# Optimization experiments

Measured on AMD Instinct MI355X. Metric: run time of the kernel, lower is better.

The kernel has to match this reference:

```python
import jax, jax.numpy as jnp
import numpy as np

N_NODES = 50000
N_EDGES = 800000
IN_F = 191
H1, C1 = 16, 16   # conv1: heads=16, out=16, concat -> 256
H2, C2 = 8, 3     # conv2: heads=8, out=3, concat=False -> mean


def _glorot(key, shape):
    fan = shape[0] + shape[-1] if len(shape) == 2 else sum(shape)
    s = jnp.sqrt(6.0 / fan)
    return jax.random.uniform(key, shape, jnp.float32, -s, s)


def setup_inputs() -> dict:
    key = jax.random.key(0)
    ks = jax.random.split(key, 16)
    x = jax.random.normal(ks[0], (N_NODES, IN_F), jnp.float32)
    edge_index = jax.random.randint(ks[1], (2, N_EDGES), 0, N_NODES)
    edge_attr = jax.random.normal(ks[2], (N_EDGES, 1), jnp.float32)
    return {
        "x": x, "edge_index": edge_index, "edge_attr": edge_attr,
        "W1": _glorot(ks[3], (IN_F, H1 * C1)),
        "We1": _glorot(ks[4], (1, H1 * C1)),
        "a_src1": _glorot(ks[5], (H1, C1)),
        "a_dst1": _glorot(ks[6], (H1, C1)),
        "a_edge1": _glorot(ks[7], (H1, C1)),
        "b1": jnp.zeros((H1 * C1,), jnp.float32),
        "W2": _glorot(ks[8], (H1 * C1, H2 * C2)),
        "We2": _glorot(ks[9], (1, H2 * C2)),
        "a_src2": _glorot(ks[10], (H2, C2)),
        "a_dst2": _glorot(ks[11], (H2, C2)),
        "a_edge2": _glorot(ks[12], (H2, C2)),
        "b2": jnp.zeros((C2,), jnp.float32),
    }


def gat_conv(x, src, dst, edge_attr, W, We, a_src, a_dst, a_edge, bias, H, C, concat):
    # x: [N, F]; src/dst: [E'] (self loops already appended); edge_attr: [E', De]
    N = x.shape[0]
    xl = (x @ W).reshape(N, H, C)                       # [N,H,C]
    e = (edge_attr @ We).reshape(-1, H, C)              # [E',H,C]
    alpha_src = (xl * a_src).sum(-1)                    # [N,H]
    alpha_dst = (xl * a_dst).sum(-1)                    # [N,H]
    alpha_e = (e * a_edge).sum(-1)                      # [E',H]
    alpha = alpha_src[src] + alpha_dst[dst] + alpha_e   # [E',H]
    alpha = jax.nn.leaky_relu(alpha, 0.2)
    # softmax over incoming edges per destination node
    m = jax.ops.segment_max(alpha, dst, num_segments=N)
    alpha = jnp.exp(alpha - m[dst])
    den = jax.ops.segment_sum(alpha, dst, num_segments=N)
    alpha = alpha / (den[dst] + 1e-16)
    out = jax.ops.segment_sum(alpha[:, :, None] * xl[src], dst, num_segments=N)  # [N,H,C]
    if concat:
        return out.reshape(N, H * C) + bias
    return out.mean(axis=1) + bias


def reference(x, edge_index, edge_attr, W1, We1, a_src1, a_dst1, a_edge1, b1,
              W2, We2, a_src2, a_dst2, a_edge2, b2):
    N = x.shape[0]
    # add self loops (PyG default, edge_attr fill_value='mean')
    loop = jnp.arange(N)
    src = jnp.concatenate([edge_index[0], loop])
    dst = jnp.concatenate([edge_index[1], loop])
    ea_mean = edge_attr.mean(axis=0, keepdims=True)
    ea = jnp.concatenate([edge_attr, jnp.broadcast_to(ea_mean, (N, edge_attr.shape[1]))], axis=0)

    h = gat_conv(x, src, dst, ea, W1, We1, a_src1, a_dst1, a_edge1, b1, H1, C1, True)
    h = jax.nn.elu(h)
    h = gat_conv(h, src, dst, ea, W2, We2, a_src2, a_dst2, a_edge2, b2, H2, C2, False)
    h = jax.nn.elu(h)
    return h
```

## Files before the change

### kernel.cpp

```cpp
#include <hip/hip_runtime.h>
#include <math.h>
#include <stdint.h>

#define N_NODES 50000
#define N_EDGES 800000
#define N_TOT   850000
#define IN_F    191
#define F1      256
#define NH1     16
#define NC1     16
#define F2      24
#define NH2     8
#define NC2     3
#define KP      192
#define MPAD    50048
#define NCVT_X  (MPAD * 24)
#define NCVT_W  (F1 * 24)

typedef __attribute__((ext_vector_type(8))) short bf16x8;
typedef __attribute__((ext_vector_type(4))) float f32x4;

#define GLL16(g, s) __builtin_amdgcn_global_load_lds( \
    (const __attribute__((address_space(1))) void*)(g), \
    (__attribute__((address_space(3))) void*)(s), 16, 0, 0)

__device__ __forceinline__ float lrelu(float x) { return x > 0.f ? x : 0.2f * x; }

__device__ __forceinline__ uint16_t f2bf1(float f) {
    uint32_t u = __float_as_uint(f);
    return (uint16_t)((u + 0x7fffu + ((u >> 16) & 1u)) >> 16);
}
__device__ __forceinline__ uint16_t f2bf(float f, float* back) {
    uint32_t u = __float_as_uint(f);
    uint32_t r = (u + 0x7fffu + ((u >> 16) & 1u)) >> 16;
    *back = __uint_as_float(r << 16);
    return (uint16_t)r;
}
__device__ __forceinline__ void bf2f2(uint32_t u, float* lo, float* hi) {
    *lo = __uint_as_float(u << 16);
    *hi = __uint_as_float(u & 0xffff0000u);
}

__global__ void k_hist(const int* __restrict__ ei, int* counts) {
    int e = blockIdx.x * blockDim.x + threadIdx.x;
    if (e < N_EDGES) atomicAdd(&counts[ei[N_EDGES + e]], 1);
}

__global__ void k_easum(const float* __restrict__ ea, float* scalars) {
    __shared__ float wsums[4];
    int t = threadIdx.x;
    float v = 0.f;
    for (int e = blockIdx.x * 256 + t; e < N_EDGES; e += 256 * 256) v += ea[e];
    #pragma unroll
    for (int off = 32; off >= 1; off >>= 1) v += __shfl_xor(v, off);
    if ((t & 63) == 0) wsums[t >> 6] = v;
    __syncthreads();
    if (t == 0) atomicAdd(&scalars[25], wsums[0] + wsums[1] + wsums[2] + wsums[3]);
}

__global__ void k_wedot(const float* __restrict__ We1, const float* __restrict__ ae1,
                        const float* __restrict__ We2, const float* __restrict__ ae2,
                        float* scalars) {
    int t = threadIdx.x;
    if (t < NH1) {
        float s = 0.f;
        for (int c = 0; c < NC1; c++) s += We1[t * NC1 + c] * ae1[t * NC1 + c];
        scalars[1 + t] = s;
    } else if (t < NH1 + NH2) {
        int h = t - NH1;
        float s = 0.f;
        for (int c = 0; c < NC2; c++) s += We2[h * NC2 + c] * ae2[h * NC2 + c];
        scalars[17 + h] = s;
    } else if (t == 63) {
        scalars[0] = scalars[25] / (float)N_EDGES;
    }
}

__global__ __launch_bounds__(1024) void k_scan1(const int* __restrict__ counts,
                                                int* rowptr, int* bsums) {
    __shared__ int wsum[16];
    int t = threadIdx.x;
    int lane = t & 63, w = t >> 6;
    int i = blockIdx.x * 1024 + t;
    int v = (i < N_NODES) ? counts[i] + 1 : 0;
    int incl = v;
    #pragma unroll
    for (int off = 1; off < 64; off <<= 1) {
        int u = __shfl_up(incl, off);
        if (lane >= off) incl += u;
    }
    if (lane == 63) wsum[w] = incl;
    __syncthreads();
    int woff = 0;
    #pragma unroll
    for (int k = 0; k < 16; k++) woff += (k < w) ? wsum[k] : 0;
    if (i < N_NODES) rowptr[i] = woff + incl - v;
    if (t == 1023) bsums[blockIdx.x] = woff + incl;
}

__global__ __launch_bounds__(1024) void k_scan2(int* rowptr, int* cursor,
                                                const int* __restrict__ bsums) {
    __shared__ int off_s;
    int b = blockIdx.x, t = threadIdx.x;
    if (t == 0) {
        int o = 0;
        for (int k = 0; k < b; k++) o += bsums[k];
        off_s = o;
        if (b == 48) rowptr[N_NODES] = o + bsums[48];
    }
    __syncthreads();
    int i = b * 1024 + t;
    if (i < N_NODES) {
        int r = rowptr[i] + off_s;
        rowptr[i] = r;
        cursor[i] = r;
    }
}

__global__ void k_scatter(const int* __restrict__ ei, const float* __restrict__ ea,
                          const float* __restrict__ scalars, int* cursor,
                          uint2* __restrict__ csr) {
    int i = blockIdx.x * blockDim.x + threadIdx.x;
    if (i < N_EDGES) {
        int s = ei[i], d = ei[N_EDGES + i];
        int pos = atomicAdd(&cursor[d], 1);
        csr[pos] = make_uint2((uint32_t)s, __float_as_uint(ea[i]));
    } else if (i < N_TOT) {
        int n = i - N_EDGES;
        int pos = atomicAdd(&cursor[n], 1);
        csr[pos] = make_uint2((uint32_t)n, __float_as_uint(scalars[0]));
    }
}

__global__ void k_cvt(const float* __restrict__ x, const float* __restrict__ W1,
                      uint16_t* __restrict__ xh, uint16_t* __restrict__ xl,
                      uint16_t* __restrict__ wht, uint16_t* __restrict__ wlt) {
    int idx = blockIdx.x * 256 + threadIdx.x;
    if (idx < NCVT_X) {
        int row = idx / 24, kw = idx - row * 24;
        int k0 = kw * 8;
        uint16_t hv[8], lv[8];
        #pragma unroll
        for (int j = 0; j < 8; j++) {
            int k = k0 + j;
            float v = (row < N_NODES && k < IN_F) ? x[(size_t)row * IN_F + k] : 0.f;
            float hf;
            hv[j] = f2bf(v, &hf);
            lv[j] = f2bf1(v - hf);
        }
        *(uint4*)(xh + (size_t)row * KP + k0) = *(const uint4*)hv;
        *(uint4*)(xl + (size_t)row * KP + k0) = *(const uint4*)lv;
    } else if (idx < NCVT_X + NCVT_W) {
        int id2 = idx - NCVT_X;
        int col = id2 / 24, kw = id2 - col * 24;
        int k0 = kw * 8;
        uint16_t hv[8], lv[8];
        #pragma unroll
        for (int j = 0; j < 8; j++) {
            int k = k0 + j;
            float v = (k < IN_F) ? W1[(size_t)k * F1 + col] : 0.f;
            float hf;
            hv[j] = f2bf(v, &hf);
            lv[j] = f2bf1(v - hf);
        }
        *(uint4*)(wht + (size_t)col * KP + k0) = *(const uint4*)hv;
        *(uint4*)(wlt + (size_t)col * KP + k0) = *(const uint4*)lv;
    }
}

__global__ __launch_bounds__(256) void k_gemm1_mfma(const uint16_t* __restrict__ xh,
        const uint16_t* __restrict__ xl, const uint16_t* __restrict__ wht,
        const uint16_t* __restrict__ wlt, uint16_t* __restrict__ xl1b) {
    __shared__ uint16_t lds[4 * 8 * 64 * 8];
    const int t = threadIdx.x;
    const int l = t & 63, w = t >> 6;
    const int wm = w >> 1, wn = w & 1;
    const int m0 = blockIdx.x * 128;
    const int n0 = blockIdx.y * 128;
    const int lr = l & 15, lk = l >> 4;

    uint16_t* ldsAh = lds;
    uint16_t* ldsAl = lds + 8 * 64 * 8;
    uint16_t* ldsBh = lds + 2 * 8 * 64 * 8;
    uint16_t* ldsBl = lds + 3 * 8 * 64 * 8;

    f32x4 acc[4][4];
    #pragma unroll
    for (int i = 0; i < 4; i++)
        #pragma unroll
        for (int j = 0; j < 4; j++)
            acc[i][j] = (f32x4){0.f, 0.f, 0.f, 0.f};

    for (int ks = 0; ks < 6; ks++) {
        const int kb = ks * 32 + lk * 8;
        #pragma unroll
        for (int ii = 0; ii < 2; ii++) {
            const int f = 2 * w + ii;
            const uint16_t* sAh = xh  + (size_t)(m0 + f * 16 + lr) * KP + kb;
            const uint16_t* sAl = xl  + (size_t)(m0 + f * 16 + lr) * KP + kb;
            const uint16_t* sBh = wht + (size_t)(n0 + f * 16 + lr) * KP + kb;
            const uint16_t* sBl = wlt + (size_t)(n0 + f * 16 + lr) * KP + kb;
            GLL16(sAh, ldsAh + f * 512);
            GLL16(sAl, ldsAl + f * 512);
            GLL16(sBh, ldsBh + f * 512);
            GLL16(sBl, ldsBl + f * 512);
        }
        __syncthreads();
        bf16x8 ah[4], al[4];
        #pragma unroll
        for (int i = 0; i < 4; i++) {
            const int f = wm * 4 + i;
            ah[i] = *(const bf16x8*)(ldsAh + (f * 64 + l) * 8);
            al[i] = *(const bf16x8*)(ldsAl + (f * 64 + l) * 8);
        }
        #pragma unroll
        for (int j = 0; j < 4; j++) {
            const int g = wn * 4 + j;
            bf16x8 bh = *(const bf16x8*)(ldsBh + (g * 64 + l) * 8);
            bf16x8 bl = *(const bf16x8*)(ldsBl + (g * 64 + l) * 8);
            #pragma unroll
            for (int i = 0; i < 4; i++) {
                acc[i][j] = __builtin_amdgcn_mfma_f32_16x16x32_bf16(ah[i], bh, acc[i][j], 0, 0, 0);
                acc[i][j] = __builtin_amdgcn_mfma_f32_16x16x32_bf16(ah[i], bl, acc[i][j], 0, 0, 0);
                acc[i][j] = __builtin_amdgcn_mfma_f32_16x16x32_bf16(al[i], bh, acc[i][j], 0, 0, 0);
            }
        }
        __syncthreads();
    }
    #pragma unroll
    for (int i = 0; i < 4; i++) {
        const int gm_base = m0 + wm * 64 + i * 16 + lk * 4;
        #pragma unroll
        for (int r = 0; r < 4; r++) {
            const int gm = gm_base + r;
            if (gm < N_NODES) {
                #pragma unroll
                for (int j = 0; j < 4; j++) {
                    const int gn = n0 + wn * 64 + j * 16 + lr;
                    xl1b[(size_t)gm * F1 + gn] = f2bf1(acc[i][j][r]);
                }
            }
        }
    }
}

__global__ void k_alphas1(const uint16_t* __restrict__ xl1b, const float* __restrict__ a_src,
                          const float* __restrict__ a_dst,
                          float* __restrict__ asrc, float* __restrict__ adst) {
    int idx = blockIdx.x * blockDim.x + threadIdx.x;
    if (idx >= N_NODES * NH1) return;
    int h = idx & 15;
    const uint4* xp = (const uint4*)(xl1b + (size_t)idx * 16);
    uint4 u0 = xp[0], u1 = xp[1];
    uint32_t us[8] = {u0.x, u0.y, u0.z, u0.w, u1.x, u1.y, u1.z, u1.w};
    float as = 0.f, ad = 0.f;
    #pragma unroll
    for (int q = 0; q < 8; q++) {
        float lo, hi;
        bf2f2(us[q], &lo, &hi);
        as += lo * a_src[h * 16 + 2 * q] + hi * a_src[h * 16 + 2 * q + 1];
        ad += lo * a_dst[h * 16 + 2 * q] + hi * a_dst[h * 16 + 2 * q + 1];
    }
    asrc[idx] = as;
    adst[idx] = ad;
}

__global__ __launch_bounds__(256) void k_agg1(const int* __restrict__ rowptr,
        const uint2* __restrict__ csr,
        const uint16_t* __restrict__ xl1b, const float* __restrict__ asrc,
        const float* __restrict__ adst, const float* __restrict__ scalars,
        const float* __restrict__ b1, uint16_t* __restrict__ h1b) {
    int node = blockIdx.x * 4 + (threadIdx.x >> 6);
    int lane = threadIdx.x & 63;
    int eg = lane >> 4, h = lane & 15;
    int r0 = rowptr[node], r1 = rowptr[node + 1];
    float ad = adst[node * 16 + h];
    float wd = scalars[1 + h];
    float den = 0.f;
    float acc[16];
    #pragma unroll
    for (int c = 0; c < 16; c++) acc[c] = 0.f;
    for (int j = r0 + eg; j < r1; j += 4) {
        uint2 pk = csr[j];
        int s = (int)pk.x;
        float a = lrelu(asrc[s * 16 + h] + ad + __uint_as_float(pk.y) * wd);
        float wgt = __expf(a);
        den += wgt;
        const uint4* xp = (const uint4*)(xl1b + (size_t)s * F1 + h * 16);
        uint4 u0 = xp[0], u1 = xp[1];
        float lo, hi;
        bf2f2(u0.x, &lo, &hi); acc[0] += wgt * lo;  acc[1] += wgt * hi;
        bf2f2(u0.y, &lo, &hi); acc[2] += wgt * lo;  acc[3] += wgt * hi;
        bf2f2(u0.z, &lo, &hi); acc[4] += wgt * lo;  acc[5] += wgt * hi;
        bf2f2(u0.w, &lo, &hi); acc[6] += wgt * lo;  acc[7] += wgt * hi;
        bf2f2(u1.x, &lo, &hi); acc[8] += wgt * lo;  acc[9] += wgt * hi;
        bf2f2(u1.y, &lo, &hi); acc[10] += wgt * lo; acc[11] += wgt * hi;
        bf2f2(u1.z, &lo, &hi); acc[12] += wgt * lo; acc[13] += wgt * hi;
        bf2f2(u1.w, &lo, &hi); acc[14] += wgt * lo; acc[15] += wgt * hi;
    }
    den += __shfl_xor(den, 16);
    den += __shfl_xor(den, 32);
    float inv = 1.f / (den + 1e-16f);
    #pragma unroll
    for (int c = 0; c < 16; c++) {
        acc[c] += __shfl_xor(acc[c], 16);
        acc[c] += __shfl_xor(acc[c], 32);
    }
    if (eg == 0) {
        uint32_t pk[8];
        #pragma unroll
        for (int q = 0; q < 8; q++) {
            float v0 = acc[2 * q] * inv + b1[h * 16 + 2 * q];
            float v1 = acc[2 * q + 1] * inv + b1[h * 16 + 2 * q + 1];
            v0 = v0 > 0.f ? v0 : expm1f(v0);
            v1 = v1 > 0.f ? v1 : expm1f(v1);
            pk[q] = (uint32_t)f2bf1(v0) | ((uint32_t)f2bf1(v1) << 16);
        }
        uint4* op = (uint4*)(h1b + (size_t)node * F1 + h * 16);
        op[0] = make_uint4(pk[0], pk[1], pk[2], pk[3]);
        op[1] = make_uint4(pk[4], pk[5], pk[6], pk[7]);
    }
}

__global__ __launch_bounds__(256) void k_layer2(const uint16_t* __restrict__ h1b,
        const float* __restrict__ W2, const float* __restrict__ a_src,
        const float* __restrict__ a_dst, uint16_t* __restrict__ xl2b,
        float* __restrict__ asrc, float* __restrict__ adst) {
    __shared__ float W2s[F2][258];
    int t = threadIdx.x;
    for (int i = t; i < 256 * F2; i += 256) {
        int k = i / F2, c = i - k * F2;
        W2s[c][k] = W2[i];
    }
    __syncthreads();
    int idx = blockIdx.x * 256 + t;
    if (idx >= N_NODES * NH2) return;
    int n = idx >> 3, h = idx & 7;
    int c0 = h * 3;
    const uint4* hp = (const uint4*)(h1b + (size_t)n * F1);
    float a0 = 0.f, a1 = 0.f, a2 = 0.f;
    #pragma unroll 4
    for (int q = 0; q < 32; q++) {
        uint4 u = hp[q];
        float f[8];
        bf2f2(u.x, &f[0], &f[1]);
        bf2f2(u.y, &f[2], &f[3]);
        bf2f2(u.z, &f[4], &f[5]);
        bf2f2(u.w, &f[6], &f[7]);
        #pragma unroll
        for (int j = 0; j < 8; j++) {
            int k = q * 8 + j;
            a0 += f[j] * W2s[c0][k];
            a1 += f[j] * W2s[c0 + 1][k];
            a2 += f[j] * W2s[c0 + 2][k];
        }
    }
    uint2 pk;
    pk.x = (uint32_t)f2bf1(a0) | ((uint32_t)f2bf1(a1) << 16);
    pk.y = (uint32_t)f2bf1(a2);
    *(uint2*)(xl2b + (size_t)idx * 4) = pk;
    asrc[idx] = a0 * a_src[h * 3 + 0] + a1 * a_src[h * 3 + 1] + a2 * a_src[h * 3 + 2];
    adst[idx] = a0 * a_dst[h * 3 + 0] + a1 * a_dst[h * 3 + 1] + a2 * a_dst[h * 3 + 2];
}

__global__ __launch_bounds__(256) void k_agg2(const int* __restrict__ rowptr,
        const uint2* __restrict__ csr,
        const uint16_t* __restrict__ xl2b, const float* __restrict__ asrc,
        const float* __restrict__ adst, const float* __restrict__ scalars,
        const float* __restrict__ b2, float* __restrict__ out) {
    int node = blockIdx.x * 4 + (threadIdx.x >> 6);
    int lane = threadIdx.x & 63;
    int eg = lane >> 3, h = lane & 7;
    int r0 = rowptr[node], r1 = rowptr[node + 1];
    float ad = adst[node * 8 + h];
    float wd = scalars[17 + h];
    float den = 0.f, a0 = 0.f, a1 = 0.f, a2 = 0.f;
    for (int j = r0 + eg; j < r1; j += 8) {
        uint2 pk = csr[j];
        int s = (int)pk.x;
        float a = lrelu(asrc[s * 8 + h] + ad + __uint_as_float(pk.y) * wd);
        float wgt = __expf(a);
        den += wgt;
        const uint2* xp = (const uint2*)(xl2b + ((size_t)s * 8 + h) * 4);
        uint2 u = xp[0];
        float x0, x1, x2, dummy;
        bf2f2(u.x, &x0, &x1);
        bf2f2(u.y, &x2, &dummy);
        a0 += wgt * x0;
        a1 += wgt * x1;
        a2 += wgt * x2;
    }
    den += __shfl_xor(den, 8); den += __shfl_xor(den, 16); den += __shfl_xor(den, 32);
    float inv = 1.f / (den + 1e-16f);
    a0 += __shfl_xor(a0, 8); a0 += __shfl_xor(a0, 16); a0 += __shfl_xor(a0, 32);
    a1 += __shfl_xor(a1, 8); a1 += __shfl_xor(a1, 16); a1 += __shfl_xor(a1, 32);
    a2 += __shfl_xor(a2, 8); a2 += __shfl_xor(a2, 16); a2 += __shfl_xor(a2, 32);
    a0 *= inv; a1 *= inv; a2 *= inv;
    a0 += __shfl_xor(a0, 1); a0 += __shfl_xor(a0, 2); a0 += __shfl_xor(a0, 4);
    a1 += __shfl_xor(a1, 1); a1 += __shfl_xor(a1, 2); a1 += __shfl_xor(a1, 4);
    a2 += __shfl_xor(a2, 1); a2 += __shfl_xor(a2, 2); a2 += __shfl_xor(a2, 4);
    if (lane == 0) {
        float v0 = a0 * 0.125f + b2[0];
        float v1 = a1 * 0.125f + b2[1];
        float v2 = a2 * 0.125f + b2[2];
        out[node * 3 + 0] = v0 > 0.f ? v0 : expm1f(v0);
        out[node * 3 + 1] = v1 > 0.f ? v1 : expm1f(v1);
        out[node * 3 + 2] = v2 > 0.f ? v2 : expm1f(v2);
    }
}

extern "C" void kernel_launch(void* const* d_in, const int* in_sizes, int n_in,
                              void* d_out, int out_size, void* d_ws, size_t ws_size,
                              hipStream_t stream) {
    const float* x       = (const float*)d_in[0];
    const int*   ei      = (const int*)d_in[1];
    const float* ea      = (const float*)d_in[2];
    const float* W1      = (const float*)d_in[3];
    const float* We1     = (const float*)d_in[4];
    const float* a_src1  = (const float*)d_in[5];
    const float* a_dst1  = (const float*)d_in[6];
    const float* a_edge1 = (const float*)d_in[7];
    const float* b1      = (const float*)d_in[8];
    const float* W2      = (const float*)d_in[9];
    const float* We2     = (const float*)d_in[10];
    const float* a_src2  = (const float*)d_in[11];
    const float* a_dst2  = (const float*)d_in[12];
    const float* a_edge2 = (const float*)d_in[13];
    const float* b2      = (const float*)d_in[14];
    float* out = (float*)d_out;

    char* ws = (char*)d_ws;
    size_t off = 0;
    auto alloc = [&](size_t nbytes) -> void* {
        void* p = ws + off;
        off = (off + nbytes + 255) & ~(size_t)255;
        return p;
    };
    uint16_t* xl1b = (uint16_t*)alloc((size_t)N_NODES * F1 * 2);
    uint16_t* h1b  = (uint16_t*)alloc((size_t)N_NODES * F1 * 2);
    float* asrc1   = (float*)alloc((size_t)N_NODES * NH1 * 4);
    float* adst1   = (float*)alloc((size_t)N_NODES * NH1 * 4);
    uint16_t* xl2b = (uint16_t*)alloc((size_t)N_NODES * 32 * 2);
    float* asrc2   = (float*)alloc((size_t)N_NODES * NH2 * 4);
    float* adst2   = (float*)alloc((size_t)N_NODES * NH2 * 4);
    int*   counts  = (int*)alloc((size_t)N_NODES * 4);
    int*   rowptr  = (int*)alloc((size_t)(N_NODES + 1) * 4);
    int*   cursor  = (int*)alloc((size_t)N_NODES * 4);
    int*   bsums   = (int*)alloc(64 * 4);
    uint2* csr     = (uint2*)alloc((size_t)N_TOT * 8);
    float* scalars = (float*)alloc(128);
    uint16_t* wht  = (uint16_t*)alloc((size_t)F1 * KP * 2);
    uint16_t* wlt  = (uint16_t*)alloc((size_t)F1 * KP * 2);
    uint16_t* xh   = (uint16_t*)alloc((size_t)MPAD * KP * 2);
    uint16_t* xlo  = (uint16_t*)alloc((size_t)MPAD * KP * 2);

    hipMemsetAsync(counts, 0, (size_t)N_NODES * 4, stream);
    hipMemsetAsync(scalars, 0, 128, stream);
    hipLaunchKernelGGL(k_hist, dim3((N_EDGES + 255) / 256), dim3(256), 0, stream,
                       ei, counts);
    hipLaunchKernelGGL(k_easum, dim3(256), dim3(256), 0, stream, ea, scalars);
    hipLaunchKernelGGL(k_wedot, dim3(1), dim3(64), 0, stream,
                       We1, a_edge1, We2, a_edge2, scalars);
    hipLaunchKernelGGL(k_scan1, dim3(49), dim3(1024), 0, stream, counts, rowptr, bsums);
    hipLaunchKernelGGL(k_scan2, dim3(49), dim3(1024), 0, stream, rowptr, cursor, bsums);
    hipLaunchKernelGGL(k_scatter, dim3((N_TOT + 255) / 256), dim3(256), 0, stream,
                       ei, ea, scalars, cursor, csr);
    hipLaunchKernelGGL(k_cvt, dim3((NCVT_X + NCVT_W + 255) / 256), dim3(256), 0, stream,
                       x, W1, xh, xlo, wht, wlt);
    hipLaunchKernelGGL(k_gemm1_mfma, dim3(MPAD / 128, 2), dim3(256), 0, stream,
                       xh, xlo, wht, wlt, xl1b);
    hipLaunchKernelGGL(k_alphas1, dim3((N_NODES * NH1 + 255) / 256), dim3(256), 0, stream,
                       xl1b, a_src1, a_dst1, asrc1, adst1);
    hipLaunchKernelGGL(k_agg1, dim3(N_NODES / 4), dim3(256), 0, stream,
                       rowptr, csr, xl1b, asrc1, adst1, scalars, b1, h1b);
    hipLaunchKernelGGL(k_layer2, dim3((N_NODES * NH2 + 255) / 256), dim3(256), 0, stream,
                       h1b, W2, a_src2, a_dst2, xl2b, asrc2, adst2);
    hipLaunchKernelGGL(k_agg2, dim3(N_NODES / 4), dim3(256), 0, stream,
                       rowptr, csr, xl2b, asrc2, adst2, scalars, b2, out);
}
```

Baseline: 327.8 us.

## Slice layer-1 features into 32-column planes and aggregate per slice for cache locality

Stores the layer-1 transformed features and hidden output as eight [N,32] bf16 slices, and runs aggregation as eight passes over edges, one per slice. Each pass's random gathers hit a small working set that can stay cached. The GEMM is retiled to 64-row blocks covering all 256 columns and writes the sliced layout; alphas and layer-2 readers are adapted. The trade-off is that CSR and attention inputs are reread eight times and each gather is narrower.

```diff
diff --git a/kernel.cpp b/kernel.cpp
--- a/kernel.cpp
+++ b/kernel.cpp
@@ -170,19 +170,15 @@
 
 __global__ __launch_bounds__(256) void k_gemm1_mfma(const uint16_t* __restrict__ xh,
         const uint16_t* __restrict__ xl, const uint16_t* __restrict__ wht,
-        const uint16_t* __restrict__ wlt, uint16_t* __restrict__ xl1b) {
-    __shared__ uint16_t lds[4 * 8 * 64 * 8];
+        const uint16_t* __restrict__ wlt, uint16_t* __restrict__ xl1s) {
+    __shared__ uint16_t Ah[4 * 64 * 8];
+    __shared__ uint16_t Al[4 * 64 * 8];
+    __shared__ uint16_t Bh[16 * 64 * 8];
+    __shared__ uint16_t Bl[16 * 64 * 8];
     const int t = threadIdx.x;
     const int l = t & 63, w = t >> 6;
-    const int wm = w >> 1, wn = w & 1;
-    const int m0 = blockIdx.x * 128;
-    const int n0 = blockIdx.y * 128;
+    const int m0 = blockIdx.x * 64;
     const int lr = l & 15, lk = l >> 4;
-
-    uint16_t* ldsAh = lds;
-    uint16_t* ldsAl = lds + 8 * 64 * 8;
-    uint16_t* ldsBh = lds + 2 * 8 * 64 * 8;
-    uint16_t* ldsBl = lds + 3 * 8 * 64 * 8;
 
     f32x4 acc[4][4];
     #pragma unroll
@@ -194,63 +190,69 @@
     for (int ks = 0; ks < 6; ks++) {
         const int kb = ks * 32 + lk * 8;
         #pragma unroll
-        for (int ii = 0; ii < 2; ii++) {
-            const int f = 2 * w + ii;
-            const uint16_t* sAh = xh  + (size_t)(m0 + f * 16 + lr) * KP + kb;
-            const uint16_t* sAl = xl  + (size_t)(m0 + f * 16 + lr) * KP + kb;
-            const uint16_t* sBh = wht + (size_t)(n0 + f * 16 + lr) * KP + kb;
-            const uint16_t* sBl = wlt + (size_t)(n0 + f * 16 + lr) * KP + kb;
-            GLL16(sAh, ldsAh + f * 512);
-            GLL16(sAl, ldsAl + f * 512);
-            GLL16(sBh, ldsBh + f * 512);
-            GLL16(sBl, ldsBl + f * 512);
+        for (int ii = 0; ii < 10; ii++) {
+            const int idx = w * 10 + ii;
+            if (idx < 8) {
+                const int f = idx >> 1;
+                const uint16_t* src = ((idx & 1) ? xl : xh) + (size_t)(m0 + f * 16 + lr) * KP + kb;
+                uint16_t* dst = ((idx & 1) ? Al : Ah) + f * 512;
+                GLL16(src, dst);
+            } else {
+                const int tt = idx - 8;
+                const int g = tt >> 1;
+                const uint16_t* src = ((tt & 1) ? wlt : wht) + (size_t)(g * 16 + lr) * KP + kb;
+                uint16_t* dst = ((tt & 1) ? Bl : Bh) + g * 512;
+                GLL16(src, dst);
+            }
         }
         __syncthreads();
         bf16x8 ah[4], al[4];
         #pragma unroll
         for (int i = 0; i < 4; i++) {
-            const int f = wm * 4 + i;
-            ah[i] = *(const bf16x8*)(ldsAh + (f * 64 + l) * 8);
-            al[i] = *(const bf16x8*)(ldsAl + (f * 64 + l) * 8);
-        }
-        #pragma unroll
-        for (int j = 0; j < 4; j++) {
-            const int g = wn * 4 + j;
-            bf16x8 bh = *(const bf16x8*)(ldsBh + (g * 64 + l) * 8);
-            bf16x8 bl = *(const bf16x8*)(ldsBl + (g * 64 + l) * 8);
+            ah[i] = *(const bf16x8*)(Ah + (i * 64 + l) * 8);
+            al[i] = *(const bf16x8*)(Al + (i * 64 + l) * 8);
+        }
+        #pragma unroll
+        for (int gq = 0; gq < 4; gq++) {
+            const int g = w * 4 + gq;
+            bf16x8 bh = *(const bf16x8*)(Bh + (g * 64 + l) * 8);
+            bf16x8 bl = *(const bf16x8*)(Bl + (g * 64 + l) * 8);
             #pragma unroll
             for (int i = 0; i < 4; i++) {
-                acc[i][j] = __builtin_amdgcn_mfma_f32_16x16x32_bf16(ah[i], bh, acc[i][j], 0, 0, 0);
-                acc[i][j] = __builtin_amdgcn_mfma_f32_16x16x32_bf16(ah[i], bl, acc[i][j], 0, 0, 0);
-                acc[i][j] = __builtin_amdgcn_mfma_f32_16x16x32_bf16(al[i], bh, acc[i][j], 0, 0, 0);
+                acc[i][gq] = __builtin_amdgcn_mfma_f32_16x16x32_bf16(ah[i], bh, acc[i][gq], 0, 0, 0);
+                acc[i][gq] = __builtin_amdgcn_mfma_f32_16x16x32_bf16(ah[i], bl, acc[i][gq], 0, 0, 0);
+                acc[i][gq] = __builtin_amdgcn_mfma_f32_16x16x32_bf16(al[i], bh, acc[i][gq], 0, 0, 0);
             }
         }
         __syncthreads();
     }
     #pragma unroll
     for (int i = 0; i < 4; i++) {
-        const int gm_base = m0 + wm * 64 + i * 16 + lk * 4;
         #pragma unroll
         for (int r = 0; r < 4; r++) {
-            const int gm = gm_base + r;
+            const int gm = m0 + i * 16 + lk * 4 + r;
             if (gm < N_NODES) {
                 #pragma unroll
-                for (int j = 0; j < 4; j++) {
-                    const int gn = n0 + wn * 64 + j * 16 + lr;
-                    xl1b[(size_t)gm * F1 + gn] = f2bf1(acc[i][j][r]);
+                for (int gq = 0; gq < 4; gq++) {
+                    const int gn = (w * 4 + gq) * 16 + lr;
+                    const int p = gn >> 5, c32 = gn & 31;
+                    xl1s[((size_t)p * N_NODES + gm) * 32 + c32] = f2bf1(acc[i][gq][r]);
                 }
             }
         }
     }
 }
 
-__global__ void k_alphas1(const uint16_t* __restrict__ xl1b, const float* __restrict__ a_src,
+__global__ void k_alphas1(const uint16_t* __restrict__ xl1s, const float* __restrict__ a_src,
                           const float* __restrict__ a_dst,
-                          float* __restrict__ asrc, float* __restrict__ adst) {
+                          float* __restrict__ asrc1s, float* __restrict__ adst1s) {
     int idx = blockIdx.x * blockDim.x + threadIdx.x;
     if (idx >= N_NODES * NH1) return;
-    int h = idx & 15;
-    const uint4* xp = (const uint4*)(xl1b + (size_t)idx * 16);
+    int p = idx / (N_NODES * 2);
+    int rem = idx - p * (N_NODES * 2);
+    int n = rem >> 1, hsub = rem & 1;
+    int h = p * 2 + hsub;
+    const uint4* xp = (const uint4*)(xl1s + ((size_t)p * N_NODES + n) * 32 + hsub * 16);
     uint4 u0 = xp[0], u1 = xp[1];
     uint32_t us[8] = {u0.x, u0.y, u0.z, u0.w, u1.x, u1.y, u1.z, u1.w};
     float as = 0.f, ad = 0.f;
@@ -261,68 +263,53 @@
         as += lo * a_src[h * 16 + 2 * q] + hi * a_src[h * 16 + 2 * q + 1];
         ad += lo * a_dst[h * 16 + 2 * q] + hi * a_dst[h * 16 + 2 * q + 1];
     }
-    asrc[idx] = as;
-    adst[idx] = ad;
+    asrc1s[idx] = as;
+    adst1s[idx] = ad;
 }
 
 __global__ __launch_bounds__(256) void k_agg1(const int* __restrict__ rowptr,
         const uint2* __restrict__ csr,
-        const uint16_t* __restrict__ xl1b, const float* __restrict__ asrc,
-        const float* __restrict__ adst, const float* __restrict__ scalars,
-        const float* __restrict__ b1, uint16_t* __restrict__ h1b) {
-    int node = blockIdx.x * 4 + (threadIdx.x >> 6);
-    int lane = threadIdx.x & 63;
-    int eg = lane >> 4, h = lane & 15;
-    int r0 = rowptr[node], r1 = rowptr[node + 1];
-    float ad = adst[node * 16 + h];
-    float wd = scalars[1 + h];
-    float den = 0.f;
-    float acc[16];
-    #pragma unroll
-    for (int c = 0; c < 16; c++) acc[c] = 0.f;
+        const uint16_t* __restrict__ xl1s, const float* __restrict__ asrc1s,
+        const float* __restrict__ adst1s, const float* __restrict__ scalars,
+        const float* __restrict__ b1, uint16_t* __restrict__ h1s) {
+    const int p = blockIdx.y;
+    const int node = blockIdx.x * 4 + (threadIdx.x >> 6);
+    const int lane = threadIdx.x & 63;
+    const int eg = lane >> 4, cc = lane & 15;
+    const int hsub = cc >> 3;
+    const int r0 = rowptr[node], r1 = rowptr[node + 1];
+    const uint16_t* slice = xl1s + (size_t)p * N_NODES * 32;
+    const float* asrc_p = asrc1s + (size_t)p * N_NODES * 2;
+    float ad = adst1s[(size_t)p * N_NODES * 2 + node * 2 + hsub];
+    float wd = scalars[1 + p * 2 + hsub];
+    float den = 0.f, acc0 = 0.f, acc1 = 0.f;
     for (int j = r0 + eg; j < r1; j += 4) {
         uint2 pk = csr[j];
         int s = (int)pk.x;
-        float a = lrelu(asrc[s * 16 + h] + ad + __uint_as_float(pk.y) * wd);
+        float a = lrelu(asrc_p[s * 2 + hsub] + ad + __uint_as_float(pk.y) * wd);
         float wgt = __expf(a);
         den += wgt;
-        const uint4* xp = (const uint4*)(xl1b + (size_t)s * F1 + h * 16);
-        uint4 u0 = xp[0], u1 = xp[1];
+        uint32_t u = *(const uint32_t*)(slice + (size_t)s * 32 + cc * 2);
         float lo, hi;
-        bf2f2(u0.x, &lo, &hi); acc[0] += wgt * lo;  acc[1] += wgt * hi;
-        bf2f2(u0.y, &lo, &hi); acc[2] += wgt * lo;  acc[3] += wgt * hi;
-        bf2f2(u0.z, &lo, &hi); acc[4] += wgt * lo;  acc[5] += wgt * hi;
-        bf2f2(u0.w, &lo, &hi); acc[6] += wgt * lo;  acc[7] += wgt * hi;
-        bf2f2(u1.x, &lo, &hi); acc[8] += wgt * lo;  acc[9] += wgt * hi;
-        bf2f2(u1.y, &lo, &hi); acc[10] += wgt * lo; acc[11] += wgt * hi;
-        bf2f2(u1.z, &lo, &hi); acc[12] += wgt * lo; acc[13] += wgt * hi;
-        bf2f2(u1.w, &lo, &hi); acc[14] += wgt * lo; acc[15] += wgt * hi;
-    }
-    den += __shfl_xor(den, 16);
-    den += __shfl_xor(den, 32);
-    float inv = 1.f / (den + 1e-16f);
-    #pragma unroll
-    for (int c = 0; c < 16; c++) {
-        acc[c] += __shfl_xor(acc[c], 16);
-        acc[c] += __shfl_xor(acc[c], 32);
-    }
+        bf2f2(u, &lo, &hi);
+        acc0 += wgt * lo;
+        acc1 += wgt * hi;
+    }
+    den  += __shfl_xor(den, 16);  den  += __shfl_xor(den, 32);
+    acc0 += __shfl_xor(acc0, 16); acc0 += __shfl_xor(acc0, 32);
+    acc1 += __shfl_xor(acc1, 16); acc1 += __shfl_xor(acc1, 32);
     if (eg == 0) {
-        uint32_t pk[8];
-        #pragma unroll
-        for (int q = 0; q < 8; q++) {
-            float v0 = acc[2 * q] * inv + b1[h * 16 + 2 * q];
-            float v1 = acc[2 * q + 1] * inv + b1[h * 16 + 2 * q + 1];
-            v0 = v0 > 0.f ? v0 : expm1f(v0);
-            v1 = v1 > 0.f ? v1 : expm1f(v1);
-            pk[q] = (uint32_t)f2bf1(v0) | ((uint32_t)f2bf1(v1) << 16);
-        }
-        uint4* op = (uint4*)(h1b + (size_t)node * F1 + h * 16);
-        op[0] = make_uint4(pk[0], pk[1], pk[2], pk[3]);
-        op[1] = make_uint4(pk[4], pk[5], pk[6], pk[7]);
-    }
-}
-
-__global__ __launch_bounds__(256) void k_layer2(const uint16_t* __restrict__ h1b,
+        float inv = 1.f / (den + 1e-16f);
+        float v0 = acc0 * inv + b1[p * 32 + 2 * cc];
+        float v1 = acc1 * inv + b1[p * 32 + 2 * cc + 1];
+        v0 = v0 > 0.f ? v0 : expm1f(v0);
+        v1 = v1 > 0.f ? v1 : expm1f(v1);
+        uint32_t pk = (uint32_t)f2bf1(v0) | ((uint32_t)f2bf1(v1) << 16);
+        *(uint32_t*)(h1s + ((size_t)p * N_NODES + node) * 32 + 2 * cc) = pk;
+    }
+}
+
+__global__ __launch_bounds__(256) void k_layer2(const uint16_t* __restrict__ h1s,
         const float* __restrict__ W2, const float* __restrict__ a_src,
         const float* __restrict__ a_dst, uint16_t* __restrict__ xl2b,
         float* __restrict__ asrc, float* __restrict__ adst) {
@@ -337,22 +324,25 @@
     if (idx >= N_NODES * NH2) return;
     int n = idx >> 3, h = idx & 7;
     int c0 = h * 3;
-    const uint4* hp = (const uint4*)(h1b + (size_t)n * F1);
     float a0 = 0.f, a1 = 0.f, a2 = 0.f;
-    #pragma unroll 4
-    for (int q = 0; q < 32; q++) {
-        uint4 u = hp[q];
-        float f[8];
-        bf2f2(u.x, &f[0], &f[1]);
-        bf2f2(u.y, &f[2], &f[3]);
-        bf2f2(u.z, &f[4], &f[5]);
-        bf2f2(u.w, &f[6], &f[7]);
-        #pragma unroll
-        for (int j = 0; j < 8; j++) {
-            int k = q * 8 + j;
-            a0 += f[j] * W2s[c0][k];
-            a1 += f[j] * W2s[c0 + 1][k];
-            a2 += f[j] * W2s[c0 + 2][k];
+    #pragma unroll
+    for (int p = 0; p < 8; p++) {
+        const uint4* hp = (const uint4*)(h1s + ((size_t)p * N_NODES + n) * 32);
+        #pragma unroll
+        for (int q = 0; q < 4; q++) {
+            uint4 u = hp[q];
+            float f[8];
+            bf2f2(u.x, &f[0], &f[1]);
+            bf2f2(u.y, &f[2], &f[3]);
+            bf2f2(u.z, &f[4], &f[5]);
+            bf2f2(u.w, &f[6], &f[7]);
+            #pragma unroll
+            for (int j = 0; j < 8; j++) {
+                int k = p * 32 + q * 8 + j;
+                a0 += f[j] * W2s[c0][k];
+                a1 += f[j] * W2s[c0 + 1][k];
+                a2 += f[j] * W2s[c0 + 2][k];
+            }
         }
     }
     uint2 pk;
@@ -436,23 +426,23 @@
         off = (off + nbytes + 255) & ~(size_t)255;
         return p;
     };
-    uint16_t* xl1b = (uint16_t*)alloc((size_t)N_NODES * F1 * 2);
-    uint16_t* h1b  = (uint16_t*)alloc((size_t)N_NODES * F1 * 2);
-    float* asrc1   = (float*)alloc((size_t)N_NODES * NH1 * 4);
-    float* adst1   = (float*)alloc((size_t)N_NODES * NH1 * 4);
-    uint16_t* xl2b = (uint16_t*)alloc((size_t)N_NODES * 32 * 2);
-    float* asrc2   = (float*)alloc((size_t)N_NODES * NH2 * 4);
-    float* adst2   = (float*)alloc((size_t)N_NODES * NH2 * 4);
-    int*   counts  = (int*)alloc((size_t)N_NODES * 4);
-    int*   rowptr  = (int*)alloc((size_t)(N_NODES + 1) * 4);
-    int*   cursor  = (int*)alloc((size_t)N_NODES * 4);
-    int*   bsums   = (int*)alloc(64 * 4);
-    uint2* csr     = (uint2*)alloc((size_t)N_TOT * 8);
-    float* scalars = (float*)alloc(128);
-    uint16_t* wht  = (uint16_t*)alloc((size_t)F1 * KP * 2);
-    uint16_t* wlt  = (uint16_t*)alloc((size_t)F1 * KP * 2);
-    uint16_t* xh   = (uint16_t*)alloc((size_t)MPAD * KP * 2);
-    uint16_t* xlo  = (uint16_t*)alloc((size_t)MPAD * KP * 2);
+    uint16_t* xl1s  = (uint16_t*)alloc((size_t)8 * N_NODES * 32 * 2);
+    uint16_t* h1s   = (uint16_t*)alloc((size_t)8 * N_NODES * 32 * 2);
+    float* asrc1s   = (float*)alloc((size_t)N_NODES * NH1 * 4);
+    float* adst1s   = (float*)alloc((size_t)N_NODES * NH1 * 4);
+    uint16_t* xl2b  = (uint16_t*)alloc((size_t)N_NODES * 32 * 2);
+    float* asrc2    = (float*)alloc((size_t)N_NODES * NH2 * 4);
+    float* adst2    = (float*)alloc((size_t)N_NODES * NH2 * 4);
+    int*   counts   = (int*)alloc((size_t)N_NODES * 4);
+    int*   rowptr   = (int*)alloc((size_t)(N_NODES + 1) * 4);
+    int*   cursor   = (int*)alloc((size_t)N_NODES * 4);
+    int*   bsums    = (int*)alloc(64 * 4);
+    uint2* csr      = (uint2*)alloc((size_t)N_TOT * 8);
+    float* scalars  = (float*)alloc(128);
+    uint16_t* wht   = (uint16_t*)alloc((size_t)F1 * KP * 2);
+    uint16_t* wlt   = (uint16_t*)alloc((size_t)F1 * KP * 2);
+    uint16_t* xh    = (uint16_t*)alloc((size_t)MPAD * KP * 2);
+    uint16_t* xlo   = (uint16_t*)alloc((size_t)MPAD * KP * 2);
 
     hipMemsetAsync(counts, 0, (size_t)N_NODES * 4, stream);
     hipMemsetAsync(scalars, 0, 128, stream);
@@ -467,14 +457,14 @@
                        ei, ea, scalars, cursor, csr);
     hipLaunchKernelGGL(k_cvt, dim3((NCVT_X + NCVT_W + 255) / 256), dim3(256), 0, stream,
                        x, W1, xh, xlo, wht, wlt);
-    hipLaunchKernelGGL(k_gemm1_mfma, dim3(MPAD / 128, 2), dim3(256), 0, stream,
-                       xh, xlo, wht, wlt, xl1b);
+    hipLaunchKernelGGL(k_gemm1_mfma, dim3(MPAD / 64), dim3(256), 0, stream,
+                       xh, xlo, wht, wlt, xl1s);
     hipLaunchKernelGGL(k_alphas1, dim3((N_NODES * NH1 + 255) / 256), dim3(256), 0, stream,
-                       xl1b, a_src1, a_dst1, asrc1, adst1);
-    hipLaunchKernelGGL(k_agg1, dim3(N_NODES / 4), dim3(256), 0, stream,
-                       rowptr, csr, xl1b, asrc1, adst1, scalars, b1, h1b);
+                       xl1s, a_src1, a_dst1, asrc1s, adst1s);
+    hipLaunchKernelGGL(k_agg1, dim3(N_NODES / 4, 8), dim3(256), 0, stream,
+                       rowptr, csr, xl1s, asrc1s, adst1s, scalars, b1, h1s);
     hipLaunchKernelGGL(k_layer2, dim3((N_NODES * NH2 + 255) / 256), dim3(256), 0, stream,
-                       h1b, W2, a_src2, a_dst2, xl2b, asrc2, adst2);
+                       h1s, W2, a_src2, a_dst2, xl2b, asrc2, adst2);
     hipLaunchKernelGGL(k_agg2, dim3(N_NODES / 4), dim3(256), 0, stream,
                        rowptr, csr, xl2b, asrc2, adst2, scalars, b2, out);
 }
```

Result: slower. 499.3 us (+52.3%).
